# Kernel optimization log

Hardware: AMD Instinct MI355X
Metric: run time of the kernel (lower is better)

The kernel has to match this reference:

```python
import jax, jax.numpy as jnp
import numpy as np
from jax import lax

BETA = 0.9      # membrane decay
THRESH = 1.0    # spike threshold


def setup_inputs() -> dict:
    key = jax.random.key(0)
    k1, k2, k3, k4 = jax.random.split(key, 4)
    B, C, T = 64, 1, 128
    N, CLASSES = 4096, 10
    x = jax.random.normal(k1, (B, C, T), dtype=jnp.float32)
    W_in = jax.random.normal(k2, (N, C), dtype=jnp.float32)
    # scale recurrent weights so the reservoir doesn't saturate every step
    W_res = jax.random.normal(k3, (N, N), dtype=jnp.float32) / jnp.sqrt(jnp.float32(N))
    W_out = jax.random.normal(k4, (CLASSES, N), dtype=jnp.float32) / jnp.sqrt(jnp.float32(N))
    return {"x": x, "W_in": W_in, "W_res": W_res, "W_out": W_out}


def reference(x, W_in, W_res, W_out):
    # x: [B, C, T]; W_in: [N, C]; W_res: [N, N]; W_out: [classes, N]
    B, C, T = x.shape
    N = W_res.shape[0]
    classes = W_out.shape[0]
    dt = x.dtype

    def step(carry, x_t):
        v_r, s_r, v_c = carry            # [B,N], [B,N], [B,classes]
        # reservoir LIF: leak + input current + recurrent current
        cur = x_t @ W_in.T + s_r @ W_res.T          # [B, N]
        v_r = BETA * v_r + cur
        s_new = (v_r >= THRESH).astype(dt)          # hard threshold spikes
        v_r = v_r * (1.0 - s_new)                   # reset-to-zero on spike
        # classifier LIF readout
        v_c = BETA * v_c + s_new @ W_out.T          # [B, classes]
        s_c = (v_c >= THRESH).astype(dt)
        v_c = v_c * (1.0 - s_c)
        return (v_r, s_new, v_c), s_c

    xs = jnp.moveaxis(x, 2, 0)  # [T, B, C]
    init = (jnp.zeros((B, N), dt), jnp.zeros((B, N), dt), jnp.zeros((B, classes), dt))
    _, out_spikes = lax.scan(step, init, xs)        # [T, B, classes]
    spike_counts = out_spikes.sum(axis=0)           # [B, classes]
    return spike_counts
```

## Files before the change

kernel.cpp:

```cpp
#include <hip/hip_runtime.h>

#define N_NEUR 4096
#define B_SZ   64
#define T_STEPS 128
#define N_CLS  10

typedef double d4v __attribute__((ext_vector_type(4)));
typedef int    i4v __attribute__((ext_vector_type(4)));
typedef long   l2v __attribute__((ext_vector_type(2)));


__device__ inline int korder2(int map, int khi, int e) {
    return map ? ((khi << 3) | e)
               : (((e >> 2) << 4) | (khi << 2) | (e & 3));
}

__global__ void kernProbe3(int* __restrict__ combo_out) {
    int l = threadIdx.x;
    int khi = l >> 4, c = l & 15;
    int best = -1;
    for (int cb = 0; cb < 8; ++cb) {
        int am = cb & 1, bm = (cb >> 1) & 1, dmap = (cb >> 2) & 1;
        unsigned long long au = 0, bu = 0;
        #pragma unroll
        for (int e = 0; e < 8; ++e) {
            int ka = korder2(am, khi, e);
            int kb = korder2(bm, khi, e);
            int aval = ((c * 5 + ka * 3) % 51) - 25;
            int bval = ((kb * 7 + c * 13) % 51) - 25;
            au |= (unsigned long long)(unsigned char)(char)aval << (8 * e);
            bu |= (unsigned long long)(unsigned char)(char)bval << (8 * e);
        }
        i4v d = {0, 0, 0, 0};
        d = __builtin_amdgcn_mfma_i32_16x16x32_i8((long)au, (long)bu, d, 0, 0, 0);
        bool ok = true;
        #pragma unroll
        for (int r = 0; r < 4; ++r) {
            int q = (l >> 4) * 4 + r;
            int di = dmap ? c : q;
            int dj = dmap ? q : c;
            int ref = 0;
            for (int k = 0; k < 32; ++k)
                ref += (((di * 5 + k * 3) % 51) - 25) * (((k * 7 + dj * 13) % 51) - 25);
            ok = ok && (d[r] == ref);
        }
        unsigned long long m = __ballot(ok);
        if (m == ~0ull && best < 0) best = cb;
    }
    if (l == 0) combo_out[3] = (best < 0) ? 0 : best;
}

__global__ __launch_bounds__(256) void kernS(const float* __restrict__ W, unsigned* __restrict__ mx) {
    unsigned m = 0;
    for (size_t i = (size_t)blockIdx.x * blockDim.x + threadIdx.x;
         i < (size_t)N_NEUR * N_NEUR; i += (size_t)gridDim.x * blockDim.x)
        m = max(m, __float_as_uint(fabsf(W[i])));
    for (int off = 32; off > 0; off >>= 1)
        m = max(m, (unsigned)__shfl_down((int)m, off, 64));
    if ((threadIdx.x & 63) == 0) atomicMax(mx, m);
}

__global__ void kernSc(const unsigned* __restrict__ mx, int* __restrict__ combo) {
    float m = __uint_as_float(*mx);
    int s = 26;
    if (m > 1e-30f) {
        s = (int)floorf(log2f(8.3e6f / m));
        while (ldexpf(m, s) > 8.3e6f) --s;
        while (ldexpf(m, s + 1) <= 8.3e6f) ++s;
    }
    combo[2] = s;
}

__global__ __launch_bounds__(256) void kernP3(const float* __restrict__ W,
                                              char* __restrict__ Wf,
                                              const int* __restrict__ combo_p) {
    const int am = combo_p[3] & 1;
    const int sc = combo_p[2];
    const int nt = blockIdx.x;
    const int lane = threadIdx.x & 63, wv = threadIdx.x >> 6;
    const int khi = lane >> 4, ai = lane & 15;
    const float* wrow = W + (size_t)(nt * 16 + ai) * N_NEUR;
    for (int kt = wv; kt < 64; kt += 4) {
        unsigned long long p0[2] = {0, 0}, p1[2] = {0, 0}, p2[2] = {0, 0};
        #pragma unroll
        for (int half = 0; half < 2; ++half) {
            #pragma unroll
            for (int e = 0; e < 8; ++e) {
                int kk = kt * 64 + half * 32 + korder2(am, khi, e);
                float w = wrow[kk];
                int q = (int)rintf(ldexpf(w, sc));
                int b0 = (int)(char)(q & 255);  int r1 = (q - b0) >> 8;
                int b1 = (int)(char)(r1 & 255); int b2 = (r1 - b1) >> 8;
                p0[half] |= (unsigned long long)(unsigned char)(char)b0 << (8 * e);
                p1[half] |= (unsigned long long)(unsigned char)(char)b1 << (8 * e);
                p2[half] |= (unsigned long long)(unsigned char)(char)b2 << (8 * e);
            }
        }
        size_t base = (((size_t)nt * 64 + kt) * 3) * 1024 + (size_t)lane * 16;
        *(l2v*)(Wf + base)        = (l2v){(long)p0[0], (long)p0[1]};
        *(l2v*)(Wf + base + 1024) = (l2v){(long)p1[0], (long)p1[1]};
        *(l2v*)(Wf + base + 2048) = (l2v){(long)p2[0], (long)p2[1]};
    }
}

__global__ __launch_bounds__(256) void kernI3m(const float* __restrict__ x,
                                               const float* __restrict__ Win,
                                               double* __restrict__ vr,
                                               unsigned* __restrict__ m0) {
    int idx = blockIdx.x * 256 + threadIdx.x;
    int b = idx & 63, n = idx >> 6;
    double v = (double)x[b * T_STEPS] * (double)Win[n];
    bool sp = (v >= 1.0);
    vr[idx] = sp ? 0.0 : v;
    if (sp)
        __hip_atomic_fetch_or(&m0[b * 256 + (n >> 4)], 1u << (n & 15),
                              __ATOMIC_RELAXED, __HIP_MEMORY_SCOPE_AGENT);
}

__device__ __forceinline__ unsigned long long expand8(unsigned w, int khi, int bm) {
    unsigned byte8;
    if (bm) byte8 = (w >> (khi * 8)) & 0xFFu;
    else    byte8 = ((w >> (khi * 4)) & 0xFu) | (((w >> (16 + khi * 4)) & 0xFu) << 4);
    unsigned rev = __builtin_bitreverse32(byte8) >> 24;
    return (((unsigned long long)rev * 0x8040201008040201ULL)
            & 0x8080808080808080ULL) >> 7;
}

__global__ __launch_bounds__(1024) void kernLoop6(const char* __restrict__ Wf,
                                                  unsigned* __restrict__ m0,
                                                  unsigned* __restrict__ m1,
                                                  const float* __restrict__ x,
                                                  const float* __restrict__ Win,
                                                  double* __restrict__ vr,
                                                  const float* __restrict__ Wout,
                                                  double* __restrict__ vc,
                                                  double* __restrict__ counts,
                                                  double* __restrict__ P0,
                                                  double* __restrict__ P1,
                                                  const int* __restrict__ combo_p,
                                                  unsigned* __restrict__ bar) {
    __shared__ double lbuf[8][1024];
    __shared__ unsigned Lm[128 * 65];
    __shared__ unsigned char spk[1024];
    __shared__ double red[16][N_CLS];
    const int bid = blockIdx.x, tid = threadIdx.x;
    const int wave = tid >> 6, lane = tid & 63;
    const int comboI = combo_p[3];
    const int sc = combo_p[2];
    const int bm = (comboI >> 1) & 1, dmap = (comboI >> 2) & 1;
    const double inv = ldexp(1.0, -sc);
    const int khi = lane >> 4, c = lane & 15;

    l2v aR[12];
    {
        const char* ap = Wf + (((size_t)bid * 64 + (size_t)wave * 4) * 3) * 1024 + (size_t)lane * 16;
        #pragma unroll
        for (int f = 0; f < 12; ++f)
            aR[f] = *(const l2v*)(ap + f * 1024);
    }

    const int nn = bid * 16 + wave;
    const int bb = lane;
    const size_t gidx = (size_t)nn * 64 + bb;
    const double winv = (double)Win[nn];
    const int cm = ((bid & 3) << 10) + tid;
    const int b2 = bid >> 2;

    for (int t = 1; t < T_STEPS; ++t) {
        const unsigned* mp = (t & 1) ? m0 : m1;
        unsigned*       mc = (t & 1) ? m1 : m0;
        double* Pcur  = (t & 1) ? P1 : P0;
        double* Pprev = (t & 1) ? P0 : P1;

        {
            const unsigned long long* mp64 = (const unsigned long long*)mp;
            #pragma unroll
            for (int r = 0; r < 8; ++r) {
                int idx2 = r * 1024 + tid;
                unsigned long long v = __hip_atomic_load(&mp64[idx2], __ATOMIC_RELAXED,
                                                         __HIP_MEMORY_SCOPE_AGENT);
                int b = idx2 >> 7, jw = idx2 & 127;
                Lm[jw * 65 + b] = (unsigned)(v & 0xFFFFu) | ((unsigned)(v >> 32) << 16);
            }
        }
        double xin = (double)x[bb * T_STEPS + t] * winv;
        double vprev = vr[gidx];
        __syncthreads();

        unsigned swc = Lm[(cm >> 5) * 65 + b2];
        float sclass = ((swc >> (cm & 31)) & 1u) ? 1.0f : 0.0f;

        #pragma unroll
        for (int btp = 0; btp < 2; ++btp) {
            i4v acc[2][3];
            #pragma unroll
            for (int i = 0; i < 2; ++i)
                #pragma unroll
                for (int s = 0; s < 3; ++s)
                    acc[i][s] = (i4v){0, 0, 0, 0};
            #pragma unroll
            for (int kt = 0; kt < 4; ++kt) {
                int ktg = wave * 4 + kt;
                #pragma unroll
                for (int bl = 0; bl < 2; ++bl) {
                    int bcol = (btp * 2 + bl) * 16 + c;
                    unsigned w0 = Lm[(ktg * 2 + 0) * 65 + bcol];
                    unsigned w1 = Lm[(ktg * 2 + 1) * 65 + bcol];
                    long lo = (long)expand8(w0, khi, bm);
                    long hi = (long)expand8(w1, khi, bm);
                    #pragma unroll
                    for (int s = 0; s < 3; ++s) {
                        acc[bl][s] = __builtin_amdgcn_mfma_i32_16x16x32_i8(aR[kt * 3 + s][0], lo, acc[bl][s], 0, 0, 0);
                        acc[bl][s] = __builtin_amdgcn_mfma_i32_16x16x32_i8(aR[kt * 3 + s][1], hi, acc[bl][s], 0, 0, 0);
                    }
                }
            }
            double v4[2][4];
            int ix[2][4];
            #pragma unroll
            for (int bl = 0; bl < 2; ++bl) {
                int btA = btp * 2 + bl;
                #pragma unroll
                for (int r = 0; r < 4; ++r) {
                    long long qq = (long long)acc[bl][2][r] * 65536LL
                                 + (long long)acc[bl][1][r] * 256LL
                                 + (long long)acc[bl][0][r];
                    v4[bl][r] = inv * (double)qq;
                    int q = (lane >> 4) * 4 + r;
                    int di = dmap ? (lane & 15) : q;
                    int dj = dmap ? q : (lane & 15);
                    ix[bl][r] = di * 64 + btA * 16 + dj;
                }
            }
            if (wave < 8) {
                #pragma unroll
                for (int bl = 0; bl < 2; ++bl)
                    #pragma unroll
                    for (int r = 0; r < 4; ++r)
                        lbuf[wave][ix[bl][r]] = v4[bl][r];
            }
            __syncthreads();
            if (wave >= 8) {
                #pragma unroll
                for (int bl = 0; bl < 2; ++bl)
                    #pragma unroll
                    for (int r = 0; r < 4; ++r)
                        lbuf[wave - 8][ix[bl][r]] += v4[bl][r];
            }
            __syncthreads();
        }

        {
            double cur = lbuf[0][tid] + lbuf[1][tid] + lbuf[2][tid] + lbuf[3][tid]
                       + lbuf[4][tid] + lbuf[5][tid] + lbuf[6][tid] + lbuf[7][tid] + xin;
            double v = 0.9 * vprev + cur;
            bool sp = (v >= 1.0);
            vr[gidx] = sp ? 0.0 : v;
            spk[lane * 16 + wave] = sp ? 1 : 0;
        }

        {
            double part[N_CLS];
            if (sclass != 0.0f) {
                #pragma unroll
                for (int cc = 0; cc < N_CLS; ++cc)
                    part[cc] = (double)Wout[cc * N_NEUR + cm];
            } else {
                #pragma unroll
                for (int cc = 0; cc < N_CLS; ++cc) part[cc] = 0.0;
            }
            #pragma unroll
            for (int cc = 0; cc < N_CLS; ++cc) {
                double v = part[cc];
                for (int off = 32; off > 0; off >>= 1)
                    v += __shfl_down(v, off, 64);
                if (lane == 0) red[wave][cc] = v;
            }
        }
        __syncthreads();

        if (wave == 0) {
            unsigned v16 = 0;
            #pragma unroll
            for (int i = 0; i < 16; ++i) v16 |= (unsigned)spk[lane * 16 + i] << i;
            __hip_atomic_store(&mc[lane * 256 + bid], v16,
                               __ATOMIC_RELAXED, __HIP_MEMORY_SCOPE_AGENT);
            if (lane < N_CLS) {
                double tot = 0.0;
                #pragma unroll
                for (int wv = 0; wv < 16; ++wv) tot += red[wv][lane];
                atomicAdd(&Pcur[b2 * N_CLS + lane], tot);
                if (bid < B_SZ && t >= 2) {
                    double pv = __hip_atomic_load(&Pprev[bid * N_CLS + lane],
                                                  __ATOMIC_RELAXED, __HIP_MEMORY_SCOPE_AGENT);
                    double v = 0.9 * vc[bid * N_CLS + lane] + pv;
                    bool sp = (v >= 1.0);
                    vc[bid * N_CLS + lane] = sp ? 0.0 : v;
                    if (sp) counts[bid * N_CLS + lane] += 1.0;
                    __hip_atomic_store(&Pprev[bid * N_CLS + lane], 0.0,
                                       __ATOMIC_RELAXED, __HIP_MEMORY_SCOPE_AGENT);
                }
            }
        }

        __syncthreads();
        if (tid == 0) {
            asm volatile("s_waitcnt vmcnt(0)" ::: "memory");
            unsigned g = (unsigned)bid >> 4;
            unsigned old = __hip_atomic_fetch_add(&bar[32 + g * 32], 1u,
                                                  __ATOMIC_RELAXED, __HIP_MEMORY_SCOPE_AGENT);
            if ((old & 15u) == 15u)
                __hip_atomic_fetch_add(&bar[0], 1u,
                                       __ATOMIC_RELAXED, __HIP_MEMORY_SCOPE_AGENT);
            unsigned tgt = 16u * (unsigned)t;
            while (__hip_atomic_load(&bar[0], __ATOMIC_RELAXED,
                                     __HIP_MEMORY_SCOPE_AGENT) < tgt)
                __builtin_amdgcn_s_sleep(1);
        }
        __syncthreads();
        asm volatile("" ::: "memory");
    }
}

__global__ __launch_bounds__(256) void kernC2m(const unsigned* __restrict__ m1,
                                               const float* __restrict__ Wout,
                                               double* __restrict__ vc,
                                               double* __restrict__ counts,
                                               const double* __restrict__ Pp) {
    int b = blockIdx.x;
    int tid = threadIdx.x;
    if (tid < N_CLS) {
        double v = 0.9 * vc[b * N_CLS + tid] + Pp[b * N_CLS + tid];
        bool sp = (v >= 1.0);
        vc[b * N_CLS + tid] = sp ? 0.0 : v;
        if (sp) counts[b * N_CLS + tid] += 1.0;
    }
    double part[N_CLS];
    #pragma unroll
    for (int c = 0; c < N_CLS; ++c) part[c] = 0.0;
    for (int m = tid; m < N_NEUR; m += 256) {
        unsigned w = m1[b * 256 + (m >> 4)];
        if ((w >> (m & 15)) & 1u) {
            #pragma unroll
            for (int c = 0; c < N_CLS; ++c)
                part[c] += (double)Wout[c * N_NEUR + m];
        }
    }
    __shared__ double red[4][N_CLS];
    int lane = tid & 63, wv = tid >> 6;
    #pragma unroll
    for (int c = 0; c < N_CLS; ++c) {
        double v = part[c];
        for (int off = 32; off > 0; off >>= 1)
            v += __shfl_down(v, off, 64);
        if (lane == 0) red[wv][c] = v;
    }
    __syncthreads();
    if (tid < N_CLS) {
        double tot = red[0][tid] + red[1][tid] + red[2][tid] + red[3][tid];
        double v = 0.9 * vc[b * N_CLS + tid] + tot;
        bool sp = (v >= 1.0);
        vc[b * N_CLS + tid] = sp ? 0.0 : v;
        if (sp) counts[b * N_CLS + tid] += 1.0;
    }
}

__global__ void kernD(const double* __restrict__ counts, float* __restrict__ out) {
    int i = blockIdx.x * blockDim.x + threadIdx.x;
    if (i < B_SZ * N_CLS) out[i] = (float)counts[i];
}


__global__ void kernProbe(int* __restrict__ combo_out) {
    int l = threadIdx.x;
    int best = -1;
    for (int c = 0; c < 16; ++c) {
        int amap = c & 1, bmap = (c >> 1) & 1, dmap = (c >> 2) & 3;
        int ai = amap ? (l >> 2) : (l & 15);
        int ak = amap ? (l & 3)  : (l >> 4);
        int bk = bmap ? (l & 3)  : (l >> 4);
        int bj = bmap ? (l >> 2) : (l & 15);
        double a = (double)(ai * 4 + ak + 1);
        double b = (double)(bk * 16 + bj + 1);
        d4v d = {0.0, 0.0, 0.0, 0.0};
        d = __builtin_amdgcn_mfma_f64_16x16x4f64(a, b, d, 0, 0, 0);
        bool ok = true;
        #pragma unroll
        for (int r = 0; r < 4; ++r) {
            int di, dj;
            if      (dmap == 0) { di = 4 * (l >> 4) + r; dj = l & 15; }
            else if (dmap == 1) { di = l & 15; dj = 4 * (l >> 4) + r; }
            else if (dmap == 2) { di = (l >> 4) + 4 * r; dj = l & 15; }
            else                { di = l & 15; dj = (l >> 4) + 4 * r; }
            double ref = 0.0;
            for (int k = 0; k < 4; ++k)
                ref += (double)(di * 4 + k + 1) * (double)(k * 16 + dj + 1);
            ok = ok && (d[r] == ref);
        }
        unsigned long long m = __ballot(ok);
        if (m == ~0ull && best < 0) best = c;
    }
    if (l == 0) combo_out[0] = (best < 0) ? 0 : best;
}

__global__ __launch_bounds__(256) void kernP(const float* __restrict__ W,
                                             float* __restrict__ Wf,
                                             const int* __restrict__ combo_p) {
    const int combo = combo_p[0];
    const int amap = combo & 1;
    const int stripe = blockIdx.x;
    const int lane = threadIdx.x & 63;
    const int ai = amap ? (lane >> 2) : (lane & 15);
    const int ak = amap ? (lane & 3)  : (lane >> 4);
    const size_t nrow = (size_t)(stripe * 16 + ai) * N_NEUR;
    for (int q = threadIdx.x >> 6; q < 1024; q += 4)
        Wf[((size_t)stripe * 1024 + q) * 64 + lane] = W[nrow + 4 * q + ak];
}

__global__ __launch_bounds__(256) void kernI(const float* __restrict__ x,
                                             const float* __restrict__ Win,
                                             double* __restrict__ vr,
                                             float* __restrict__ sf,
                                             float* __restrict__ sT) {
    int idx = blockIdx.x * 256 + threadIdx.x;
    int b = idx & 63, n = idx >> 6;
    double v = (double)x[b * T_STEPS] * (double)Win[n];
    bool sp = (v >= 1.0);
    vr[idx] = sp ? 0.0 : v;
    float s = sp ? 1.0f : 0.0f;
    sT[idx] = s;
    sf[(size_t)(((n >> 2) * 4 + (b >> 4)) * 64) + (n & 3) * 16 + (b & 15)] = s;
}

template<bool USEWF>
__global__ __launch_bounds__(1024) void kernAB(const float* __restrict__ Wsrc,
                                               const float* __restrict__ sfp,
                                               const float* __restrict__ x,
                                               const float* __restrict__ Win,
                                               double* __restrict__ vr,
                                               float* __restrict__ sfc,
                                               float* __restrict__ sTc,
                                               const float* __restrict__ sTp,
                                               const float* __restrict__ Wout,
                                               double* __restrict__ vc,
                                               double* __restrict__ counts,
                                               const int* __restrict__ combo_p,
                                               int t) {
    __shared__ double lbuf[4][16 * 64];
    __shared__ double red[16][N_CLS];
    const int tid  = threadIdx.x;
    const int wave = tid >> 6, lane = tid & 63;

    if (blockIdx.x >= 256) {
        const int b = blockIdx.x - 256;
        double part[N_CLS];
        #pragma unroll
        for (int c = 0; c < N_CLS; ++c) part[c] = 0.0;
        for (int m = tid; m < N_NEUR; m += 1024) {
            double s = (double)sTp[(size_t)m * B_SZ + b];
            #pragma unroll
            for (int c = 0; c < N_CLS; ++c)
                part[c] = fma(s, (double)Wout[c * N_NEUR + m], part[c]);
        }
        #pragma unroll
        for (int c = 0; c < N_CLS; ++c) {
            double v = part[c];
            for (int off = 32; off > 0; off >>= 1)
                v += __shfl_down(v, off, 64);
            if (lane == 0) red[wave][c] = v;
        }
        __syncthreads();
        if (tid < N_CLS) {
            double tot = 0.0;
            #pragma unroll
            for (int wv = 0; wv < 16; ++wv) tot += red[wv][tid];
            double v = 0.9 * vc[b * N_CLS + tid] + tot;
            bool sp = (v >= 1.0);
            vc[b * N_CLS + tid] = sp ? 0.0 : v;
            if (sp) counts[b * N_CLS + tid] += 1.0;
        }
        return;
    }

    const int wb = wave & 3, wq = wave >> 2;
    const int gn0 = blockIdx.x * 16;
    const int combo = combo_p[0];
    const int amap = combo & 1, bmap = (combo >> 1) & 1, dmap = (combo >> 2) & 3;
    const int bk = bmap ? (lane & 3)  : (lane >> 4);
    const int bj = bmap ? (lane >> 2) : (lane & 15);

    d4v acc = {0.0, 0.0, 0.0, 0.0};
    const int q0 = wq * 256;
    const float* bp = sfp + (size_t)(q0 * 4 + wb) * 64 + bk * 16 + bj;

    if (USEWF) {
        const float* ap = Wsrc + ((size_t)blockIdx.x * 1024 + q0) * 64 + lane;
        for (int blk = 0; blk < 64; ++blk) {
            #pragma unroll
            for (int u = 0; u < 4; ++u) {
                double a  = (double)ap[u * 64];
                double bv = (double)bp[u * 256];
                acc = __builtin_amdgcn_mfma_f64_16x16x4f64(a, bv, acc, 0, 0, 0);
            }
            ap += 256;
            bp += 1024;
        }
    } else {
        const int ai = amap ? (lane >> 2) : (lane & 15);
        const int ak = amap ? (lane & 3)  : (lane >> 4);
        #pragma unroll 4
        for (int q = 0; q < 256; ++q) {
            double a  = (double)Wsrc[(size_t)(gn0 + ai) * N_NEUR + 4 * (q0 + q) + ak];
            double bv = (double)bp[(size_t)q * 256];
            acc = __builtin_amdgcn_mfma_f64_16x16x4f64(a, bv, acc, 0, 0, 0);
        }
    }

    {
        const int jb = 16 * wb;
        #pragma unroll
        for (int r = 0; r < 4; ++r) {
            int di, dj;
            if      (dmap == 0) { di = 4 * (lane >> 4) + r; dj = lane & 15; }
            else if (dmap == 1) { di = lane & 15; dj = 4 * (lane >> 4) + r; }
            else if (dmap == 2) { di = (lane >> 4) + 4 * r; dj = lane & 15; }
            else                { di = lane & 15; dj = (lane >> 4) + 4 * r; }
            lbuf[wq][di * 64 + jb + dj] = acc[r];
        }
    }
    __syncthreads();

    int nl = tid >> 6, b = tid & 63;
    int n = gn0 + nl;
    size_t gidx = (size_t)n * 64 + b;
    double cur = lbuf[0][tid] + lbuf[1][tid] + lbuf[2][tid] + lbuf[3][tid]
               + (double)x[b * T_STEPS + t] * (double)Win[n];
    double v = 0.9 * vr[gidx] + cur;
    bool sp = (v >= 1.0);
    vr[gidx] = sp ? 0.0 : v;
    float s = sp ? 1.0f : 0.0f;
    sTc[gidx] = s;
    sfc[(size_t)(((n >> 2) * 4 + (b >> 4)) * 64) + (n & 3) * 16 + (b & 15)] = s;
}

__global__ __launch_bounds__(256) void kernC(const float* __restrict__ sT,
                                             const float* __restrict__ Wout,
                                             double* __restrict__ vc,
                                             double* __restrict__ counts) {
    int b = blockIdx.x;
    int tid = threadIdx.x;
    double part[N_CLS];
    #pragma unroll
    for (int c = 0; c < N_CLS; ++c) part[c] = 0.0;
    for (int m = tid; m < N_NEUR; m += 256) {
        double s = (double)sT[(size_t)m * B_SZ + b];
        #pragma unroll
        for (int c = 0; c < N_CLS; ++c)
            part[c] = fma(s, (double)Wout[c * N_NEUR + m], part[c]);
    }
    __shared__ double red[4][N_CLS];
    int lane = tid & 63, wv = tid >> 6;
    #pragma unroll
    for (int c = 0; c < N_CLS; ++c) {
        double v = part[c];
        for (int off = 32; off > 0; off >>= 1)
            v += __shfl_down(v, off, 64);
        if (lane == 0) red[wv][c] = v;
    }
    __syncthreads();
    if (tid < N_CLS) {
        double tot = red[0][tid] + red[1][tid] + red[2][tid] + red[3][tid];
        double v = 0.9 * vc[b * N_CLS + tid] + tot;
        bool sp = (v >= 1.0);
        vc[b * N_CLS + tid] = sp ? 0.0 : v;
        if (sp) counts[b * N_CLS + tid] += 1.0;
    }
}

extern "C" void kernel_launch(void* const* d_in, const int* in_sizes, int n_in,
                              void* d_out, int out_size, void* d_ws, size_t ws_size,
                              hipStream_t stream) {
    const float* x    = (const float*)d_in[0];
    const float* Win  = (const float*)d_in[1];
    const float* Wres = (const float*)d_in[2];
    const float* Wout = (const float*)d_in[3];
    float* out = (float*)d_out;

    const size_t NB = (size_t)B_SZ * N_NEUR;
    char* w = (char*)d_ws;
    double* vr     = (double*)w;  w += NB * sizeof(double);
    float*  sTa    = (float*)w;   w += NB * sizeof(float);
    float*  sTb    = (float*)w;   w += NB * sizeof(float);
    float*  sf0    = (float*)w;   w += NB * sizeof(float);
    float*  sf1    = (float*)w;   w += NB * sizeof(float);
    double* vc     = (double*)w;  w += (size_t)B_SZ * N_CLS * sizeof(double);
    double* counts = (double*)w;  w += (size_t)B_SZ * N_CLS * sizeof(double);
    double* P0     = (double*)w;  w += (size_t)B_SZ * N_CLS * sizeof(double);
    double* P1     = (double*)w;  w += (size_t)B_SZ * N_CLS * sizeof(double);
    int*    combo  = (int*)w;     w += 256;
    unsigned* bar  = (unsigned*)w; w += 4096;
    float*  Wf     = (float*)w;

    size_t fixed = (size_t)(w - (char*)d_ws);
    bool use_i8 = (ws_size >= fixed + 3ull * N_NEUR * N_NEUR);
    bool use_wf = (ws_size >= fixed + (size_t)N_NEUR * N_NEUR * sizeof(float));

    hipMemsetAsync(vc, 0, 4ull * B_SZ * N_CLS * sizeof(double), stream);
    hipMemsetAsync(combo, 0, 256, stream);
    hipMemsetAsync(bar, 0, 4096, stream);

    if (use_i8) {
        char* Wfi = (char*)Wf;
        unsigned* m0 = (unsigned*)sf0;
        unsigned* m1 = (unsigned*)sf1;
        unsigned* mx = (unsigned*)(combo + 8);

        hipMemsetAsync(m0, 0, 64 * 1024, stream);
        hipMemsetAsync(m1, 0, 64 * 1024, stream);

        kernProbe3<<<dim3(1), 64, 0, stream>>>(combo);
        kernS<<<dim3(1024), 256, 0, stream>>>(Wres, mx);
        kernSc<<<dim3(1), 1, 0, stream>>>(mx, combo);
        kernP3<<<dim3(256), 256, 0, stream>>>(Wres, Wfi, combo);
        kernI3m<<<dim3(NB / 256), 256, 0, stream>>>(x, Win, vr, m0);

        kernLoop6<<<dim3(256), 1024, 0, stream>>>(Wfi, m0, m1, x, Win, vr,
                                                  Wout, vc, counts, P0, P1, combo, bar);

        kernC2m<<<dim3(B_SZ), 256, 0, stream>>>(m1, Wout, vc, counts, P1);
        kernD<<<dim3(3), 256, 0, stream>>>(counts, out);
        return;
    }

    kernProbe<<<dim3(1), 64, 0, stream>>>(combo);
    if (use_wf)
        kernP<<<dim3(256), 256, 0, stream>>>(Wres, Wf, combo);

    kernI<<<dim3(NB / 256), 256, 0, stream>>>(x, Win, vr, sf0, sTa);
    for (int t = 1; t < T_STEPS; ++t) {
        const float* sfp = (t & 1) ? sf0 : sf1;
        float*       sfc = (t & 1) ? sf1 : sf0;
        float*       sTc = (t & 1) ? sTb : sTa;
        const float* sTp = (t & 1) ? sTa : sTb;
        if (use_wf)
            kernAB<true><<<dim3(320), 1024, 0, stream>>>(Wf, sfp, x, Win, vr, sfc, sTc, sTp,
                                                         Wout, vc, counts, combo, t);
        else
            kernAB<false><<<dim3(320), 1024, 0, stream>>>(Wres, sfp, x, Win, vr, sfc, sTc, sTp,
                                                          Wout, vc, counts, combo, t);
    }
    kernC<<<dim3(B_SZ), 256, 0, stream>>>(sTb, Wout, vc, counts);
    kernD<<<dim3(3), 256, 0, stream>>>(counts, out);
}
```

Measured before the change: 3.027 ms.

## Merge MFMA batch halves, use int LDS reduction, restructure classifier readout per wave

Processes all four batch tiles in one MFMA pass, which halves the LDS cross-wave reduction rounds and their barriers. The partial sums are stored to LDS as packed int32 pairs instead of doubles, and conversion to double happens once after the reduction. The classifier readout changes from every thread loading 10 Wout values and doing 10 shuffle reductions to one wave per class that skips non-spiking neurons, each wave doing a single reduction and its own atomicAdd. In exchange, more accumulator registers are live at once, and relying on int32 packing assumes partial sums cannot overflow.

```diff
diff --git a/kernel.cpp b/kernel.cpp
--- a/kernel.cpp
+++ b/kernel.cpp
@@ -126,7 +126,7 @@
             & 0x8080808080808080ULL) >> 7;
 }
 
-__global__ __launch_bounds__(1024) void kernLoop6(const char* __restrict__ Wf,
+__global__ __launch_bounds__(1024) void kernLoop7(const char* __restrict__ Wf,
                                                   unsigned* __restrict__ m0,
                                                   unsigned* __restrict__ m1,
                                                   const float* __restrict__ x,
@@ -139,10 +139,9 @@
                                                   double* __restrict__ P1,
                                                   const int* __restrict__ combo_p,
                                                   unsigned* __restrict__ bar) {
-    __shared__ double lbuf[8][1024];
+    __shared__ int2 lbufI[8][1024];
     __shared__ unsigned Lm[128 * 65];
     __shared__ unsigned char spk[1024];
-    __shared__ double red[16][N_CLS];
     const int bid = blockIdx.x, tid = threadIdx.x;
     const int wave = tid >> 6, lane = tid & 63;
     const int comboI = combo_p[3];
@@ -163,8 +162,8 @@
     const int bb = lane;
     const size_t gidx = (size_t)nn * 64 + bb;
     const double winv = (double)Win[nn];
-    const int cm = ((bid & 3) << 10) + tid;
     const int b2 = bid >> 2;
+    const int mbase = (bid & 3) << 10;
 
     for (int t = 1; t < T_STEPS; ++t) {
         const unsigned* mp = (t & 1) ? m0 : m1;
@@ -187,96 +186,100 @@
         double vprev = vr[gidx];
         __syncthreads();
 
-        unsigned swc = Lm[(cm >> 5) * 65 + b2];
-        float sclass = ((swc >> (cm & 31)) & 1u) ? 1.0f : 0.0f;
-
-        #pragma unroll
-        for (int btp = 0; btp < 2; ++btp) {
-            i4v acc[2][3];
-            #pragma unroll
-            for (int i = 0; i < 2; ++i)
+        i4v acc[4][3];
+        #pragma unroll
+        for (int i = 0; i < 4; ++i)
+            #pragma unroll
+            for (int s = 0; s < 3; ++s)
+                acc[i][s] = (i4v){0, 0, 0, 0};
+        #pragma unroll
+        for (int kt = 0; kt < 4; ++kt) {
+            int ktg = wave * 4 + kt;
+            #pragma unroll
+            for (int bl = 0; bl < 4; ++bl) {
+                int bcol = bl * 16 + c;
+                unsigned w0 = Lm[(ktg * 2 + 0) * 65 + bcol];
+                unsigned w1 = Lm[(ktg * 2 + 1) * 65 + bcol];
+                long lo = (long)expand8(w0, khi, bm);
+                long hi = (long)expand8(w1, khi, bm);
                 #pragma unroll
-                for (int s = 0; s < 3; ++s)
-                    acc[i][s] = (i4v){0, 0, 0, 0};
-            #pragma unroll
-            for (int kt = 0; kt < 4; ++kt) {
-                int ktg = wave * 4 + kt;
-                #pragma unroll
-                for (int bl = 0; bl < 2; ++bl) {
-                    int bcol = (btp * 2 + bl) * 16 + c;
-                    unsigned w0 = Lm[(ktg * 2 + 0) * 65 + bcol];
-                    unsigned w1 = Lm[(ktg * 2 + 1) * 65 + bcol];
-                    long lo = (long)expand8(w0, khi, bm);
-                    long hi = (long)expand8(w1, khi, bm);
-                    #pragma unroll
-                    for (int s = 0; s < 3; ++s) {
-                        acc[bl][s] = __builtin_amdgcn_mfma_i32_16x16x32_i8(aR[kt * 3 + s][0], lo, acc[bl][s], 0, 0, 0);
-                        acc[bl][s] = __builtin_amdgcn_mfma_i32_16x16x32_i8(aR[kt * 3 + s][1], hi, acc[bl][s], 0, 0, 0);
-                    }
+                for (int s = 0; s < 3; ++s) {
+                    acc[bl][s] = __builtin_amdgcn_mfma_i32_16x16x32_i8(aR[kt * 3 + s][0], lo, acc[bl][s], 0, 0, 0);
+                    acc[bl][s] = __builtin_amdgcn_mfma_i32_16x16x32_i8(aR[kt * 3 + s][1], hi, acc[bl][s], 0, 0, 0);
                 }
             }
-            double v4[2][4];
-            int ix[2][4];
-            #pragma unroll
-            for (int bl = 0; bl < 2; ++bl) {
-                int btA = btp * 2 + bl;
+        }
+
+        double ctot = 0.0;
+        if (wave < N_CLS) {
+            const float* wrow = Wout + (size_t)wave * N_NEUR + mbase;
+            double s = 0.0;
+            #pragma unroll
+            for (int j = 0; j < 16; ++j) {
+                unsigned wd = Lm[((mbase >> 5) + j * 2 + (lane >> 5)) * 65 + b2];
+                if ((wd >> (lane & 31)) & 1u)
+                    s += (double)wrow[j * 64 + lane];
+            }
+            for (int off = 32; off > 0; off >>= 1)
+                s += __shfl_down(s, off, 64);
+            ctot = s;
+        }
+
+        {
+            int2 pk[4][4];
+            int ix[4][4];
+            #pragma unroll
+            for (int bl = 0; bl < 4; ++bl) {
                 #pragma unroll
                 for (int r = 0; r < 4; ++r) {
-                    long long qq = (long long)acc[bl][2][r] * 65536LL
-                                 + (long long)acc[bl][1][r] * 256LL
-                                 + (long long)acc[bl][0][r];
-                    v4[bl][r] = inv * (double)qq;
+                    pk[bl][r].x = acc[bl][0][r] + acc[bl][1][r] * 256;
+                    pk[bl][r].y = acc[bl][2][r];
                     int q = (lane >> 4) * 4 + r;
                     int di = dmap ? (lane & 15) : q;
                     int dj = dmap ? q : (lane & 15);
-                    ix[bl][r] = di * 64 + btA * 16 + dj;
+                    ix[bl][r] = di * 64 + bl * 16 + dj;
                 }
             }
             if (wave < 8) {
                 #pragma unroll
-                for (int bl = 0; bl < 2; ++bl)
+                for (int bl = 0; bl < 4; ++bl)
                     #pragma unroll
                     for (int r = 0; r < 4; ++r)
-                        lbuf[wave][ix[bl][r]] = v4[bl][r];
+                        lbufI[wave][ix[bl][r]] = pk[bl][r];
             }
             __syncthreads();
             if (wave >= 8) {
                 #pragma unroll
-                for (int bl = 0; bl < 2; ++bl)
+                for (int bl = 0; bl < 4; ++bl)
                     #pragma unroll
-                    for (int r = 0; r < 4; ++r)
-                        lbuf[wave - 8][ix[bl][r]] += v4[bl][r];
+                    for (int r = 0; r < 4; ++r) {
+                        int2 tcur = lbufI[wave - 8][ix[bl][r]];
+                        tcur.x += pk[bl][r].x;
+                        tcur.y += pk[bl][r].y;
+                        lbufI[wave - 8][ix[bl][r]] = tcur;
+                    }
             }
             __syncthreads();
         }
 
         {
-            double cur = lbuf[0][tid] + lbuf[1][tid] + lbuf[2][tid] + lbuf[3][tid]
-                       + lbuf[4][tid] + lbuf[5][tid] + lbuf[6][tid] + lbuf[7][tid] + xin;
+            int s01 = 0, s2 = 0;
+            #pragma unroll
+            for (int j = 0; j < 8; ++j) {
+                int2 v2 = lbufI[j][tid];
+                s01 += v2.x;
+                s2  += v2.y;
+            }
+            double cur = inv * ((double)s01 + 65536.0 * (double)s2) + xin;
             double v = 0.9 * vprev + cur;
             bool sp = (v >= 1.0);
             vr[gidx] = sp ? 0.0 : v;
             spk[lane * 16 + wave] = sp ? 1 : 0;
         }
 
-        {
-            double part[N_CLS];
-            if (sclass != 0.0f) {
-                #pragma unroll
-                for (int cc = 0; cc < N_CLS; ++cc)
-                    part[cc] = (double)Wout[cc * N_NEUR + cm];
-            } else {
-                #pragma unroll
-                for (int cc = 0; cc < N_CLS; ++cc) part[cc] = 0.0;
-            }
-            #pragma unroll
-            for (int cc = 0; cc < N_CLS; ++cc) {
-                double v = part[cc];
-                for (int off = 32; off > 0; off >>= 1)
-                    v += __shfl_down(v, off, 64);
-                if (lane == 0) red[wave][cc] = v;
-            }
-        }
+        if (wave < N_CLS && lane == 0)
+            atomicAdd(&Pcur[b2 * N_CLS + wave], ctot);
+
         __syncthreads();
 
         if (wave == 0) {
@@ -285,21 +288,15 @@
             for (int i = 0; i < 16; ++i) v16 |= (unsigned)spk[lane * 16 + i] << i;
             __hip_atomic_store(&mc[lane * 256 + bid], v16,
                                __ATOMIC_RELAXED, __HIP_MEMORY_SCOPE_AGENT);
-            if (lane < N_CLS) {
-                double tot = 0.0;
-                #pragma unroll
-                for (int wv = 0; wv < 16; ++wv) tot += red[wv][lane];
-                atomicAdd(&Pcur[b2 * N_CLS + lane], tot);
-                if (bid < B_SZ && t >= 2) {
-                    double pv = __hip_atomic_load(&Pprev[bid * N_CLS + lane],
-                                                  __ATOMIC_RELAXED, __HIP_MEMORY_SCOPE_AGENT);
-                    double v = 0.9 * vc[bid * N_CLS + lane] + pv;
-                    bool sp = (v >= 1.0);
-                    vc[bid * N_CLS + lane] = sp ? 0.0 : v;
-                    if (sp) counts[bid * N_CLS + lane] += 1.0;
-                    __hip_atomic_store(&Pprev[bid * N_CLS + lane], 0.0,
-                                       __ATOMIC_RELAXED, __HIP_MEMORY_SCOPE_AGENT);
-                }
+            if (lane < N_CLS && bid < B_SZ && t >= 2) {
+                double pv = __hip_atomic_load(&Pprev[bid * N_CLS + lane],
+                                              __ATOMIC_RELAXED, __HIP_MEMORY_SCOPE_AGENT);
+                double v = 0.9 * vc[bid * N_CLS + lane] + pv;
+                bool sp = (v >= 1.0);
+                vc[bid * N_CLS + lane] = sp ? 0.0 : v;
+                if (sp) counts[bid * N_CLS + lane] += 1.0;
+                __hip_atomic_store(&Pprev[bid * N_CLS + lane], 0.0,
+                                   __ATOMIC_RELAXED, __HIP_MEMORY_SCOPE_AGENT);
             }
         }
 
@@ -624,7 +621,7 @@
         kernP3<<<dim3(256), 256, 0, stream>>>(Wres, Wfi, combo);
         kernI3m<<<dim3(NB / 256), 256, 0, stream>>>(x, Win, vr, m0);
 
-        kernLoop6<<<dim3(256), 1024, 0, stream>>>(Wfi, m0, m1, x, Win, vr,
+        kernLoop7<<<dim3(256), 1024, 0, stream>>>(Wfi, m0, m1, x, Win, vr,
                                                   Wout, vc, counts, P0, P1, combo, bar);
 
         kernC2m<<<dim3(B_SZ), 256, 0, stream>>>(m1, Wout, vc, counts, P1);
```

After: 3.403 ms. 1.12x slower.
